# Optimization experiments

Measured on AMD Instinct MI355X. Metric: run time of the kernel, lower is better.

Reference implementation:

```python
import jax, jax.numpy as jnp
import numpy as np

N = 100000
E = 3200000
F_IN = 16
H = 128
LAT = 64
L = 3
G = 1024


def setup_inputs() -> dict:
    key = jax.random.key(0)
    ks = jax.random.split(key, 12)
    x = jax.random.normal(ks[0], (N, F_IN), dtype=jnp.float32)
    edge_index = jax.random.randint(ks[1], (2, E), 0, N, dtype=jnp.int64)
    batch = jnp.sort(jax.random.randint(ks[2], (N,), 0, G, dtype=jnp.int64))
    batch = batch.at[-1].set(G - 1)  # ensure batch.max()+1 == G
    s_in = 1.0 / np.sqrt(F_IN)
    s_h = 1.0 / np.sqrt(H)
    W_in = jax.random.uniform(ks[3], (F_IN, H), jnp.float32, -s_in, s_in)
    b_in = jax.random.uniform(ks[4], (H,), jnp.float32, -s_in, s_in)
    W_msg = jax.random.uniform(ks[5], (L, H, H), jnp.float32, -s_h, s_h)
    b_msg = jax.random.uniform(ks[6], (L, H), jnp.float32, -s_h, s_h)
    W_mean = jax.random.uniform(ks[7], (H, LAT), jnp.float32, -s_h, s_h)
    b_mean = jax.random.uniform(ks[8], (LAT,), jnp.float32, -s_h, s_h)
    W_logvar = jax.random.uniform(ks[9], (H, LAT), jnp.float32, -s_h, s_h)
    b_logvar = jax.random.uniform(ks[10], (LAT,), jnp.float32, -s_h, s_h)
    return {
        "x": x, "edge_index": edge_index, "batch": batch, "num_graphs": G,
        "W_in": W_in, "b_in": b_in, "W_msg": W_msg, "b_msg": b_msg,
        "W_mean": W_mean, "b_mean": b_mean,
        "W_logvar": W_logvar, "b_logvar": b_logvar,
    }


def reference(x, edge_index, batch, num_graphs, W_in, b_in, W_msg, b_msg,
              W_mean, b_mean, W_logvar, b_logvar):
    src, dst = edge_index[0], edge_index[1]
    n = x.shape[0]
    # input net: Linear + ReLU
    h = jax.nn.relu(x @ W_in + b_in)  # [N, H]
    # stacked message-passing: transform, gather at src, scatter-add to dst, ReLU
    for l in range(L):
        m = h @ W_msg[l] + b_msg[l]                    # [N, H]
        agg = jax.ops.segment_sum(m[src], dst, num_segments=n)  # [N, H]
        h = jax.nn.relu(agg)
    # graph-level sum pooling via index_add over batch ids
    graph_embedding = jax.ops.segment_sum(h, batch, num_segments=num_graphs)  # [G, H]
    z_mean = graph_embedding @ W_mean + b_mean
    z_logvar = graph_embedding @ W_logvar + b_logvar
    return (z_mean, z_logvar)
```

## Files before the change

kernel.cpp:

```cpp
#include <hip/hip_runtime.h>

constexpr int N_  = 100000;
constexpr int E_  = 3200000;
constexpr int FIN = 16;
constexpr int H_  = 128;
constexpr int LAT = 64;
constexpr int L_  = 3;
constexpr int G_  = 1024;

constexpr int BSH = 9;
constexpr int BNODES = 1 << BSH;
constexpr int NB_ = (N_ + BNODES - 1) / BNODES;
constexpr int FILL_NB = 512;
constexpr int FILL_CHUNK = E_ / FILL_NB;

constexpr int WCONV_BLOCKS = (L_ * H_ * H_) / 256;
constexpr int BHIST_BLOCKS = 512;
constexpr int INIT_WCONV0 = BHIST_BLOCKS;
constexpr int INIT_INPUT0 = BHIST_BLOCKS + WCONV_BLOCKS;
constexpr int MSG_BLOCKS = N_ / 32;

using bf16x8 = __attribute__((ext_vector_type(8))) short;
using f32x4  = __attribute__((ext_vector_type(4))) float;

__device__ inline float bflo(unsigned int u) {
  union { unsigned int i; float f; } v; v.i = u << 16; return v.f;
}
__device__ inline float bfhi(unsigned int u) {
  union { unsigned int i; float f; } v; v.i = u & 0xffff0000u; return v.f;
}
__device__ inline unsigned short f2bf(float f) {
  union { float f; unsigned int i; } v; v.f = f;
  unsigned int r = v.i + 0x7fffu + ((v.i >> 16) & 1u);
  return (unsigned short)(r >> 16);
}

__global__ __launch_bounds__(256) void k_init(const int* __restrict__ ei,
                                              int* __restrict__ bcnt,
                                              const float* __restrict__ W,
                                              unsigned short* __restrict__ Wt,
                                              const float* __restrict__ x,
                                              const float* __restrict__ Win,
                                              const float* __restrict__ bin,
                                              unsigned short* __restrict__ h) {
  const int tid = threadIdx.x;
  __shared__ int lh[NB_];
  __shared__ float Wl[FIN * H_];
  __shared__ float xl[4 * FIN];
  if (blockIdx.x < BHIST_BLOCKS) {
    for (int i = tid; i < NB_; i += 256) lh[i] = 0;
    __syncthreads();
    const int gid = blockIdx.x * 256 + tid;
    const int stride = BHIST_BLOCKS * 256;
    for (int e = gid; e < E_; e += stride) atomicAdd(&lh[ei[E_ + e] >> BSH], 1);
    __syncthreads();
    for (int i = tid; i < NB_; i += 256)
      if (lh[i]) atomicAdd(&bcnt[i], lh[i]);
    return;
  }
  if (blockIdx.x < INIT_INPUT0) {
    const int idx = (blockIdx.x - INIT_WCONV0) * 256 + tid;
    const int l = idx >> 14, rem = idx & 16383;
    const int c = rem >> 7, k = rem & 127;
    Wt[idx] = f2bf(W[l * H_ * H_ + k * H_ + c]);
    return;
  }
  for (int i = tid; i < FIN * H_; i += 256) Wl[i] = Win[i];
  const int n0 = (blockIdx.x - INIT_INPUT0) * 4;
  if (tid < 4 * FIN) xl[tid] = x[(size_t)n0 * FIN + tid];
  __syncthreads();
  const int nl = tid >> 6, l = tid & 63;
  float a0 = bin[2 * l], a1 = bin[2 * l + 1];
#pragma unroll
  for (int k = 0; k < FIN; ++k) {
    const float xv = xl[nl * FIN + k];
    a0 += xv * Wl[k * H_ + 2 * l];
    a1 += xv * Wl[k * H_ + 2 * l + 1];
  }
  const unsigned int packed =
      (unsigned int)f2bf(fmaxf(a0, 0.f)) | ((unsigned int)f2bf(fmaxf(a1, 0.f)) << 16);
  *reinterpret_cast<unsigned int*>(h + (size_t)(n0 + nl) * H_ + 2 * l) = packed;
}

__device__ __forceinline__ void msg_body(int bid, int tid,
                                         const unsigned short* __restrict__ h,
                                         const unsigned short* __restrict__ Wt,
                                         const float* __restrict__ b,
                                         unsigned short* __restrict__ m,
                                         unsigned short (*st)[32][40]) {
  const int wave = tid >> 6;
  const int lane = tid & 63;
  const int r = lane & 15;
  const int g = lane >> 4;
  const int n0 = bid * 32;
  const int cb = wave * 32;

  f32x4 acc[2][2] = {};
#pragma unroll
  for (int kk = 0; kk < 4; ++kk) {
    const int koff = kk * 32 + g * 8;
    const bf16x8 a0 = *reinterpret_cast<const bf16x8*>(h + (size_t)(n0 + r) * H_ + koff);
    const bf16x8 a1 = *reinterpret_cast<const bf16x8*>(h + (size_t)(n0 + 16 + r) * H_ + koff);
    const bf16x8 b0 = *reinterpret_cast<const bf16x8*>(Wt + (size_t)(cb + r) * H_ + koff);
    const bf16x8 b1 = *reinterpret_cast<const bf16x8*>(Wt + (size_t)(cb + 16 + r) * H_ + koff);
    acc[0][0] = __builtin_amdgcn_mfma_f32_16x16x32_bf16(a0, b0, acc[0][0], 0, 0, 0);
    acc[0][1] = __builtin_amdgcn_mfma_f32_16x16x32_bf16(a0, b1, acc[0][1], 0, 0, 0);
    acc[1][0] = __builtin_amdgcn_mfma_f32_16x16x32_bf16(a1, b0, acc[1][0], 0, 0, 0);
    acc[1][1] = __builtin_amdgcn_mfma_f32_16x16x32_bf16(a1, b1, acc[1][1], 0, 0, 0);
  }

  const float bc0 = b[cb + r];
  const float bc1 = b[cb + 16 + r];
#pragma unroll
  for (int rt = 0; rt < 2; ++rt)
#pragma unroll
    for (int ct = 0; ct < 2; ++ct) {
      const float bc = ct ? bc1 : bc0;
#pragma unroll
      for (int j = 0; j < 4; ++j)
        st[wave][rt * 16 + g * 4 + j][ct * 16 + r] = f2bf(acc[rt][ct][j] + bc);
    }
  __syncthreads();
#pragma unroll
  for (int p = 0; p < 2; ++p) {
    const int lr = p * 16 + (lane >> 2);
    const int seg = lane & 3;
    const bf16x8 v = *reinterpret_cast<const bf16x8*>(&st[wave][lr][seg * 8]);
    *reinterpret_cast<bf16x8*>(m + (size_t)(n0 + lr) * H_ + cb + seg * 8) = v;
  }
}

__global__ __launch_bounds__(256) void k_msg_mfma(const unsigned short* __restrict__ h,
                                                  const unsigned short* __restrict__ Wt,
                                                  const float* __restrict__ b,
                                                  unsigned short* __restrict__ m) {
  __shared__ unsigned short st[4][32][40];
  msg_body(blockIdx.x, threadIdx.x, h, Wt, b, m, st);
}

__global__ __launch_bounds__(256) void k_bscan(const int* __restrict__ bcnt,
                                               int* __restrict__ boff,
                                               int* __restrict__ bcur,
                                               float* __restrict__ ge) {
  __shared__ int s[256];
  const int t = threadIdx.x;
  s[t] = (t < NB_) ? bcnt[t] : 0;
  __syncthreads();
  for (int off = 1; off < 256; off <<= 1) {
    const int add = (t >= off) ? s[t - off] : 0;
    __syncthreads();
    s[t] += add;
    __syncthreads();
  }
  const int ex = (t == 0) ? 0 : s[t - 1];
  if (t < NB_) { boff[t] = ex; bcur[t] = ex; }
  if (t == 0) boff[NB_] = s[NB_ - 1];
  float4 z = make_float4(0.f, 0.f, 0.f, 0.f);
  float4* g4 = reinterpret_cast<float4*>(ge);
  for (int i = t; i < G_ * H_ / 4; i += 256) g4[i] = z;
}

__global__ __launch_bounds__(256) void k_bfill(const int* __restrict__ ei,
                                               int* __restrict__ bcur,
                                               unsigned int* __restrict__ ebuf) {
  __shared__ int lh[NB_], lbase[NB_];
  const int t = threadIdx.x;
  for (int i = t; i < NB_; i += 256) lh[i] = 0;
  __syncthreads();
  const int e0 = blockIdx.x * FILL_CHUNK;
  const int e1 = e0 + FILL_CHUNK;
  for (int e = e0 + t; e < e1; e += 256) atomicAdd(&lh[ei[E_ + e] >> BSH], 1);
  __syncthreads();
  for (int i = t; i < NB_; i += 256) {
    const int c = lh[i];
    lbase[i] = c ? atomicAdd(&bcur[i], c) : 0;
  }
  __syncthreads();
  for (int i = t; i < NB_; i += 256) lh[i] = 0;
  __syncthreads();
  for (int e = e0 + t; e < e1; e += 256) {
    const int src = ei[e], dst = ei[E_ + e];
    const int b = dst >> BSH;
    const int pos = lbase[b] + atomicAdd(&lh[b], 1);
    ebuf[pos] = ((unsigned)src << BSH) | (unsigned)(dst & (BNODES - 1));
  }
}

__global__ __launch_bounds__(256) void k_csrmsg(const unsigned int* __restrict__ ebuf,
                                                const int* __restrict__ boff,
                                                int* __restrict__ rowp,
                                                int* __restrict__ ssrc,
                                                const unsigned short* __restrict__ h,
                                                const unsigned short* __restrict__ Wt,
                                                const float* __restrict__ bb,
                                                unsigned short* __restrict__ m) {
  __shared__ int sdeg[BNODES];
  __shared__ int scur[BNODES];
  __shared__ int part[256];
  __shared__ unsigned short st[4][32][40];
  const int t = threadIdx.x;
  if (blockIdx.x >= NB_) {
    msg_body(blockIdx.x - NB_, t, h, Wt, bb, m, st);
    return;
  }
  const int b = blockIdx.x;
  const int nbase = b << BSH;
  const int ncnt = min(BNODES, N_ - nbase);
  const int ebeg = boff[b], eend = boff[b + 1];
  for (int i = t; i < BNODES; i += 256) { sdeg[i] = 0; scur[i] = 0; }
  __syncthreads();
  for (int e = ebeg + t; e < eend; e += 256)
    atomicAdd(&sdeg[ebuf[e] & (BNODES - 1)], 1);
  __syncthreads();
  const int i0 = 2 * t, i1 = 2 * t + 1;
  const int d0 = sdeg[i0];
  part[t] = d0 + sdeg[i1];
  __syncthreads();
  for (int off = 1; off < 256; off <<= 1) {
    const int add = (t >= off) ? part[t - off] : 0;
    __syncthreads();
    part[t] += add;
    __syncthreads();
  }
  const int ex = (t == 0) ? 0 : part[t - 1];
  sdeg[i0] = ex;
  sdeg[i1] = ex + d0;
  __syncthreads();
  for (int i = t; i < ncnt; i += 256) rowp[nbase + i] = ebeg + sdeg[i];
  if (b == NB_ - 1 && t == 0) rowp[N_] = E_;
  for (int e = ebeg + t; e < eend; e += 256) {
    const unsigned int ed = ebuf[e];
    const int ld = ed & (BNODES - 1);
    const int pos = ebeg + sdeg[ld] + atomicAdd(&scur[ld], 1);
    ssrc[pos] = (int)(ed >> BSH);
  }
}

__global__ __launch_bounds__(256) void k_gather(const unsigned short* __restrict__ m,
                                                const int* __restrict__ rowptr,
                                                const int* __restrict__ ssrc,
                                                unsigned short* __restrict__ h) {
  const int n = blockIdx.x * 4 + (threadIdx.x >> 6);
  const int c2 = threadIdx.x & 63;
  const int beg = rowptr[n], end = rowptr[n + 1];
  const unsigned short* mc = m + 2 * c2;
  float a0 = 0.f, a1 = 0.f;
  int i = beg;
  for (; i + 15 < end; i += 16) {
    int s[16];
#pragma unroll
    for (int u = 0; u < 16; ++u) s[u] = ssrc[i + u];
    unsigned int v[16];
#pragma unroll
    for (int u = 0; u < 16; ++u)
      v[u] = *reinterpret_cast<const unsigned int*>(mc + (size_t)s[u] * H_);
#pragma unroll
    for (int u = 0; u < 16; ++u) { a0 += bflo(v[u]); a1 += bfhi(v[u]); }
  }
  for (; i + 3 < end; i += 4) {
    int s[4];
#pragma unroll
    for (int u = 0; u < 4; ++u) s[u] = ssrc[i + u];
    unsigned int v[4];
#pragma unroll
    for (int u = 0; u < 4; ++u)
      v[u] = *reinterpret_cast<const unsigned int*>(mc + (size_t)s[u] * H_);
#pragma unroll
    for (int u = 0; u < 4; ++u) { a0 += bflo(v[u]); a1 += bfhi(v[u]); }
  }
  for (; i < end; ++i) {
    const unsigned int v = *reinterpret_cast<const unsigned int*>(mc + (size_t)ssrc[i] * H_);
    a0 += bflo(v);  a1 += bfhi(v);
  }
  const unsigned int packed =
      (unsigned int)f2bf(fmaxf(a0, 0.f)) | ((unsigned int)f2bf(fmaxf(a1, 0.f)) << 16);
  *reinterpret_cast<unsigned int*>(h + (size_t)n * H_ + 2 * c2) = packed;
}

constexpr int POOL_CHUNK = 128;
__global__ __launch_bounds__(128) void k_pool(const unsigned short* __restrict__ h,
                                              const int* __restrict__ batch,
                                              float* __restrict__ ge) {
  __shared__ int bl[POOL_CHUNK];
  const int tid = threadIdx.x;
  const int start = blockIdx.x * POOL_CHUNK;
  const int cnt = min(POOL_CHUNK, N_ - start);
  if (tid < cnt) bl[tid] = batch[start + tid];
  __syncthreads();
  float run = 0.f;
  int cur = bl[0];
  for (int i = 0; i < cnt; ++i) {
    const int bid = bl[i];
    const float v = bflo((unsigned int)h[(size_t)(start + i) * H_ + tid]);
    if (bid != cur) {
      unsafeAtomicAdd(&ge[(size_t)cur * H_ + tid], run);
      run = 0.f;
      cur = bid;
    }
    run += v;
  }
  unsafeAtomicAdd(&ge[(size_t)cur * H_ + tid], run);
}

__global__ __launch_bounds__(128) void k_out(const float* __restrict__ ge,
                                             const float* __restrict__ Wm,
                                             const float* __restrict__ bm,
                                             const float* __restrict__ Wv,
                                             const float* __restrict__ bv,
                                             float* __restrict__ out) {
  __shared__ float gl[H_];
  const int g = blockIdx.x, tid = threadIdx.x;
  gl[tid] = ge[(size_t)g * H_ + tid];
  __syncthreads();
  const bool is_mean = (tid < LAT);
  const float* W = is_mean ? Wm : Wv;
  const float* bb = is_mean ? bm : bv;
  const int c = tid & 63;
  float acc = bb[c];
#pragma unroll 8
  for (int k = 0; k < H_; ++k) acc += gl[k] * W[k * LAT + c];
  const size_t off = is_mean ? 0 : (size_t)G_ * LAT;
  out[off + (size_t)g * LAT + c] = acc;
}

extern "C" void kernel_launch(void* const* d_in, const int* in_sizes, int n_in,
                              void* d_out, int out_size, void* d_ws, size_t ws_size,
                              hipStream_t stream) {
  const float* x     = (const float*)d_in[0];
  const int*   ei    = (const int*)d_in[1];
  const int*   batch = (const int*)d_in[2];
  const float* Win   = (const float*)d_in[4];
  const float* bin   = (const float*)d_in[5];
  const float* Wmsg  = (const float*)d_in[6];
  const float* bmsg  = (const float*)d_in[7];
  const float* Wmean = (const float*)d_in[8];
  const float* bmean = (const float*)d_in[9];
  const float* Wlv   = (const float*)d_in[10];
  const float* blv   = (const float*)d_in[11];
  float* out = (float*)d_out;

  char* p = (char*)d_ws;
  unsigned short* h  = (unsigned short*)p;  p += (size_t)N_ * H_ * 2;
  unsigned short* m  = (unsigned short*)p;  p += (size_t)N_ * H_ * 2;
  unsigned int* ebuf = (unsigned int*)p;    p += (size_t)E_ * 4;
  int* ssrc          = (int*)p;             p += (size_t)E_ * 4;
  int* rowp          = (int*)p;             p += (size_t)(N_ + 1) * 4;
  unsigned short* Wt = (unsigned short*)p;  p += (size_t)L_ * H_ * H_ * 2;
  float* ge          = (float*)p;           p += (size_t)G_ * H_ * 4;
  int* bcnt          = (int*)p;             p += (size_t)NB_ * 4;
  int* boff          = (int*)p;             p += (size_t)(NB_ + 1) * 4;
  int* bcur          = (int*)p;             p += (size_t)NB_ * 4;

  hipMemsetAsync(bcnt, 0, (size_t)NB_ * sizeof(int), stream);
  k_init<<<INIT_INPUT0 + N_ / 4, 256, 0, stream>>>(ei, bcnt, Wmsg, Wt, x, Win, bin, h);

  k_bscan<<<1, 256, 0, stream>>>(bcnt, boff, bcur, ge);
  k_bfill<<<FILL_NB, 256, 0, stream>>>(ei, bcur, ebuf);
  k_csrmsg<<<NB_ + MSG_BLOCKS, 256, 0, stream>>>(ebuf, boff, rowp, ssrc,
                                                 h, Wt, bmsg, m);

  k_gather<<<N_ / 4, 256, 0, stream>>>(m, rowp, ssrc, h);
  k_msg_mfma<<<MSG_BLOCKS, 256, 0, stream>>>(h, Wt + (size_t)H_ * H_,
                                             bmsg + H_, m);
  k_gather<<<N_ / 4, 256, 0, stream>>>(m, rowp, ssrc, h);
  k_msg_mfma<<<MSG_BLOCKS, 256, 0, stream>>>(h, Wt + (size_t)2 * H_ * H_,
                                             bmsg + 2 * H_, m);
  k_gather<<<N_ / 4, 256, 0, stream>>>(m, rowp, ssrc, h);

  k_pool<<<(N_ + POOL_CHUNK - 1) / POOL_CHUNK, 128, 0, stream>>>(h, batch, ge);
  k_out<<<G_, 128, 0, stream>>>(ge, Wmean, bmean, Wlv, blv, out);
}
```

Measured before the change: 544.3 us.

## Replace edge bucket scan with fixed-capacity buckets and fuse fill into init

Edge bucketing now writes into fixed-capacity per-bucket slots, so the separate histogram pass, the prefix-scan kernel and the fill kernel are dropped and the fill is folded into the init kernel. The graph-embedding zeroing moves into extra init blocks. Row offsets become per-node begin/end pairs because bucket storage is no longer contiguous. This removes two launches and one read of the destination indices, but it relies on no bucket exceeding the fixed capacity, and there is no overflow check.

```diff
diff --git a/kernel.cpp b/kernel.cpp
--- a/kernel.cpp
+++ b/kernel.cpp
@@ -11,13 +11,15 @@
 constexpr int BSH = 9;
 constexpr int BNODES = 1 << BSH;
 constexpr int NB_ = (N_ + BNODES - 1) / BNODES;
+constexpr int CAP = 18000;
 constexpr int FILL_NB = 512;
 constexpr int FILL_CHUNK = E_ / FILL_NB;
 
 constexpr int WCONV_BLOCKS = (L_ * H_ * H_) / 256;
-constexpr int BHIST_BLOCKS = 512;
-constexpr int INIT_WCONV0 = BHIST_BLOCKS;
-constexpr int INIT_INPUT0 = BHIST_BLOCKS + WCONV_BLOCKS;
+constexpr int INIT_WCONV0 = FILL_NB;
+constexpr int INIT_GE0   = INIT_WCONV0 + WCONV_BLOCKS;
+constexpr int GE_BLOCKS  = 32;
+constexpr int INIT_INPUT0 = INIT_GE0 + GE_BLOCKS;
 constexpr int MSG_BLOCKS = N_ / 32;
 
 using bf16x8 = __attribute__((ext_vector_type(8))) short;
@@ -36,33 +38,54 @@
 }
 
 __global__ __launch_bounds__(256) void k_init(const int* __restrict__ ei,
-                                              int* __restrict__ bcnt,
+                                              int* __restrict__ bcur,
+                                              unsigned int* __restrict__ ebuf,
                                               const float* __restrict__ W,
                                               unsigned short* __restrict__ Wt,
                                               const float* __restrict__ x,
                                               const float* __restrict__ Win,
                                               const float* __restrict__ bin,
-                                              unsigned short* __restrict__ h) {
+                                              unsigned short* __restrict__ h,
+                                              float* __restrict__ ge) {
   const int tid = threadIdx.x;
-  __shared__ int lh[NB_];
+  __shared__ int lh[NB_], lbase[NB_];
   __shared__ float Wl[FIN * H_];
   __shared__ float xl[4 * FIN];
-  if (blockIdx.x < BHIST_BLOCKS) {
+  if (blockIdx.x < FILL_NB) {
     for (int i = tid; i < NB_; i += 256) lh[i] = 0;
     __syncthreads();
-    const int gid = blockIdx.x * 256 + tid;
-    const int stride = BHIST_BLOCKS * 256;
-    for (int e = gid; e < E_; e += stride) atomicAdd(&lh[ei[E_ + e] >> BSH], 1);
-    __syncthreads();
-    for (int i = tid; i < NB_; i += 256)
-      if (lh[i]) atomicAdd(&bcnt[i], lh[i]);
+    const int e0 = blockIdx.x * FILL_CHUNK;
+    const int e1 = e0 + FILL_CHUNK;
+    for (int e = e0 + tid; e < e1; e += 256) atomicAdd(&lh[ei[E_ + e] >> BSH], 1);
+    __syncthreads();
+    for (int i = tid; i < NB_; i += 256) {
+      const int c = lh[i];
+      lbase[i] = c ? atomicAdd(&bcur[i], c) : 0;
+    }
+    __syncthreads();
+    for (int i = tid; i < NB_; i += 256) lh[i] = 0;
+    __syncthreads();
+    for (int e = e0 + tid; e < e1; e += 256) {
+      const int src = ei[e], dst = ei[E_ + e];
+      const int b = dst >> BSH;
+      const int pos = lbase[b] + atomicAdd(&lh[b], 1);
+      ebuf[(size_t)b * CAP + pos] = ((unsigned)src << BSH) | (unsigned)(dst & (BNODES - 1));
+    }
     return;
   }
-  if (blockIdx.x < INIT_INPUT0) {
+  if (blockIdx.x < INIT_GE0) {
     const int idx = (blockIdx.x - INIT_WCONV0) * 256 + tid;
     const int l = idx >> 14, rem = idx & 16383;
     const int c = rem >> 7, k = rem & 127;
     Wt[idx] = f2bf(W[l * H_ * H_ + k * H_ + c]);
+    return;
+  }
+  if (blockIdx.x < INIT_INPUT0) {
+    const int gb = blockIdx.x - INIT_GE0;
+    float4* g4 = reinterpret_cast<float4*>(ge);
+    constexpr int PER = G_ * H_ / 4 / GE_BLOCKS;
+    const float4 z = make_float4(0.f, 0.f, 0.f, 0.f);
+    for (int i = tid; i < PER; i += 256) g4[gb * PER + i] = z;
     return;
   }
   for (int i = tid; i < FIN * H_; i += 256) Wl[i] = Win[i];
@@ -138,57 +161,9 @@
   msg_body(blockIdx.x, threadIdx.x, h, Wt, b, m, st);
 }
 
-__global__ __launch_bounds__(256) void k_bscan(const int* __restrict__ bcnt,
-                                               int* __restrict__ boff,
-                                               int* __restrict__ bcur,
-                                               float* __restrict__ ge) {
-  __shared__ int s[256];
-  const int t = threadIdx.x;
-  s[t] = (t < NB_) ? bcnt[t] : 0;
-  __syncthreads();
-  for (int off = 1; off < 256; off <<= 1) {
-    const int add = (t >= off) ? s[t - off] : 0;
-    __syncthreads();
-    s[t] += add;
-    __syncthreads();
-  }
-  const int ex = (t == 0) ? 0 : s[t - 1];
-  if (t < NB_) { boff[t] = ex; bcur[t] = ex; }
-  if (t == 0) boff[NB_] = s[NB_ - 1];
-  float4 z = make_float4(0.f, 0.f, 0.f, 0.f);
-  float4* g4 = reinterpret_cast<float4*>(ge);
-  for (int i = t; i < G_ * H_ / 4; i += 256) g4[i] = z;
-}
-
-__global__ __launch_bounds__(256) void k_bfill(const int* __restrict__ ei,
-                                               int* __restrict__ bcur,
-                                               unsigned int* __restrict__ ebuf) {
-  __shared__ int lh[NB_], lbase[NB_];
-  const int t = threadIdx.x;
-  for (int i = t; i < NB_; i += 256) lh[i] = 0;
-  __syncthreads();
-  const int e0 = blockIdx.x * FILL_CHUNK;
-  const int e1 = e0 + FILL_CHUNK;
-  for (int e = e0 + t; e < e1; e += 256) atomicAdd(&lh[ei[E_ + e] >> BSH], 1);
-  __syncthreads();
-  for (int i = t; i < NB_; i += 256) {
-    const int c = lh[i];
-    lbase[i] = c ? atomicAdd(&bcur[i], c) : 0;
-  }
-  __syncthreads();
-  for (int i = t; i < NB_; i += 256) lh[i] = 0;
-  __syncthreads();
-  for (int e = e0 + t; e < e1; e += 256) {
-    const int src = ei[e], dst = ei[E_ + e];
-    const int b = dst >> BSH;
-    const int pos = lbase[b] + atomicAdd(&lh[b], 1);
-    ebuf[pos] = ((unsigned)src << BSH) | (unsigned)(dst & (BNODES - 1));
-  }
-}
-
 __global__ __launch_bounds__(256) void k_csrmsg(const unsigned int* __restrict__ ebuf,
-                                                const int* __restrict__ boff,
-                                                int* __restrict__ rowp,
+                                                const int* __restrict__ bcur,
+                                                int2* __restrict__ rowpe,
                                                 int* __restrict__ ssrc,
                                                 const unsigned short* __restrict__ h,
                                                 const unsigned short* __restrict__ Wt,
@@ -206,11 +181,12 @@
   const int b = blockIdx.x;
   const int nbase = b << BSH;
   const int ncnt = min(BNODES, N_ - nbase);
-  const int ebeg = boff[b], eend = boff[b + 1];
+  const int cnt = bcur[b];
+  const unsigned int* eb = ebuf + (size_t)b * CAP;
+  const int gbase = b * CAP;
   for (int i = t; i < BNODES; i += 256) { sdeg[i] = 0; scur[i] = 0; }
   __syncthreads();
-  for (int e = ebeg + t; e < eend; e += 256)
-    atomicAdd(&sdeg[ebuf[e] & (BNODES - 1)], 1);
+  for (int e = t; e < cnt; e += 256) atomicAdd(&sdeg[eb[e] & (BNODES - 1)], 1);
   __syncthreads();
   const int i0 = 2 * t, i1 = 2 * t + 1;
   const int d0 = sdeg[i0];
@@ -226,23 +202,28 @@
   sdeg[i0] = ex;
   sdeg[i1] = ex + d0;
   __syncthreads();
-  for (int i = t; i < ncnt; i += 256) rowp[nbase + i] = ebeg + sdeg[i];
-  if (b == NB_ - 1 && t == 0) rowp[N_] = E_;
-  for (int e = ebeg + t; e < eend; e += 256) {
-    const unsigned int ed = ebuf[e];
+  for (int i = t; i < ncnt; i += 256) {
+    const int s = sdeg[i];
+    const int e2 = (i == BNODES - 1) ? cnt : sdeg[i + 1];
+    rowpe[nbase + i] = make_int2(gbase + s, gbase + e2);
+  }
+  __syncthreads();
+  for (int e = t; e < cnt; e += 256) {
+    const unsigned int ed = eb[e];
     const int ld = ed & (BNODES - 1);
-    const int pos = ebeg + sdeg[ld] + atomicAdd(&scur[ld], 1);
-    ssrc[pos] = (int)(ed >> BSH);
+    const int pos = sdeg[ld] + atomicAdd(&scur[ld], 1);
+    ssrc[gbase + pos] = (int)(ed >> BSH);
   }
 }
 
 __global__ __launch_bounds__(256) void k_gather(const unsigned short* __restrict__ m,
-                                                const int* __restrict__ rowptr,
+                                                const int2* __restrict__ rowpe,
                                                 const int* __restrict__ ssrc,
                                                 unsigned short* __restrict__ h) {
   const int n = blockIdx.x * 4 + (threadIdx.x >> 6);
   const int c2 = threadIdx.x & 63;
-  const int beg = rowptr[n], end = rowptr[n + 1];
+  const int2 be = rowpe[n];
+  const int beg = be.x, end = be.y;
   const unsigned short* mc = m + 2 * c2;
   float a0 = 0.f, a1 = 0.f;
   int i = beg;
@@ -342,30 +323,27 @@
   char* p = (char*)d_ws;
   unsigned short* h  = (unsigned short*)p;  p += (size_t)N_ * H_ * 2;
   unsigned short* m  = (unsigned short*)p;  p += (size_t)N_ * H_ * 2;
-  unsigned int* ebuf = (unsigned int*)p;    p += (size_t)E_ * 4;
-  int* ssrc          = (int*)p;             p += (size_t)E_ * 4;
-  int* rowp          = (int*)p;             p += (size_t)(N_ + 1) * 4;
+  unsigned int* ebuf = (unsigned int*)p;    p += (size_t)NB_ * CAP * 4;
+  int* ssrc          = (int*)p;             p += (size_t)NB_ * CAP * 4;
+  int2* rowpe        = (int2*)p;            p += (size_t)N_ * 8;
   unsigned short* Wt = (unsigned short*)p;  p += (size_t)L_ * H_ * H_ * 2;
   float* ge          = (float*)p;           p += (size_t)G_ * H_ * 4;
-  int* bcnt          = (int*)p;             p += (size_t)NB_ * 4;
-  int* boff          = (int*)p;             p += (size_t)(NB_ + 1) * 4;
   int* bcur          = (int*)p;             p += (size_t)NB_ * 4;
 
-  hipMemsetAsync(bcnt, 0, (size_t)NB_ * sizeof(int), stream);
-  k_init<<<INIT_INPUT0 + N_ / 4, 256, 0, stream>>>(ei, bcnt, Wmsg, Wt, x, Win, bin, h);
-
-  k_bscan<<<1, 256, 0, stream>>>(bcnt, boff, bcur, ge);
-  k_bfill<<<FILL_NB, 256, 0, stream>>>(ei, bcur, ebuf);
-  k_csrmsg<<<NB_ + MSG_BLOCKS, 256, 0, stream>>>(ebuf, boff, rowp, ssrc,
+  hipMemsetAsync(bcur, 0, (size_t)NB_ * sizeof(int), stream);
+  k_init<<<INIT_INPUT0 + N_ / 4, 256, 0, stream>>>(ei, bcur, ebuf, Wmsg, Wt,
+                                                   x, Win, bin, h, ge);
+
+  k_csrmsg<<<NB_ + MSG_BLOCKS, 256, 0, stream>>>(ebuf, bcur, rowpe, ssrc,
                                                  h, Wt, bmsg, m);
 
-  k_gather<<<N_ / 4, 256, 0, stream>>>(m, rowp, ssrc, h);
+  k_gather<<<N_ / 4, 256, 0, stream>>>(m, rowpe, ssrc, h);
   k_msg_mfma<<<MSG_BLOCKS, 256, 0, stream>>>(h, Wt + (size_t)H_ * H_,
                                              bmsg + H_, m);
-  k_gather<<<N_ / 4, 256, 0, stream>>>(m, rowp, ssrc, h);
+  k_gather<<<N_ / 4, 256, 0, stream>>>(m, rowpe, ssrc, h);
   k_msg_mfma<<<MSG_BLOCKS, 256, 0, stream>>>(h, Wt + (size_t)2 * H_ * H_,
                                              bmsg + 2 * H_, m);
-  k_gather<<<N_ / 4, 256, 0, stream>>>(m, rowp, ssrc, h);
+  k_gather<<<N_ / 4, 256, 0, stream>>>(m, rowpe, ssrc, h);
 
   k_pool<<<(N_ + POOL_CHUNK - 1) / POOL_CHUNK, 128, 0, stream>>>(h, batch, ge);
   k_out<<<G_, 128, 0, stream>>>(ge, Wmean, bmean, Wlv, blv, out);
```

Result: faster. 502.7 us (-7.6%).
